# Performance work log

Measured on AMD Instinct MI355X. Metric: run time of the kernel, lower is better.

## Reference

```python
import jax, jax.numpy as jnp
import numpy as np

B, T, D, N, H = 2, 2048, 2048, 16, 128
WINDOW = 1024
SOFT_CAP = 50.0
K_MASK = -2.3819763e+38
MAX_WAVELENGTH = 10000


def apply_rope(x, positions, head_dim):
    # x: [B, T, N, H], positions: [B, T]
    fraction = 2.0 * jnp.arange(head_dim // 2, dtype=jnp.float32) / head_dim
    timescale = MAX_WAVELENGTH ** fraction                      # [H/2]
    sinusoid = positions[..., None].astype(jnp.float32) / timescale  # [B, T, H/2]
    sinusoid = sinusoid[..., None, :]                           # [B, T, 1, H/2]
    sin, cos = jnp.sin(sinusoid), jnp.cos(sinusoid)
    first, second = jnp.split(x, 2, axis=-1)
    out = jnp.concatenate([first * cos - second * sin,
                           second * cos + first * sin], axis=-1)
    return out.astype(x.dtype)


def setup_inputs() -> dict:
    key = jax.random.key(0)
    k1, k2, k3 = jax.random.split(key, 3)
    x = jax.random.normal(k1, (B, T, D), dtype=jnp.float32)
    w_qkv = jax.random.normal(k2, (3, N, D, H), dtype=jnp.float32) * (D ** -0.5)
    w_out = jax.random.normal(k3, (N, H, D), dtype=jnp.float32) * ((N * H) ** -0.5)
    segment_pos = jnp.broadcast_to(jnp.arange(T, dtype=jnp.int32), (B, T))
    # causal attention mask [B, T, S]
    causal = jnp.tril(jnp.ones((T, T), dtype=jnp.bool_))
    attn_mask = jnp.broadcast_to(causal, (B, T, T))
    return {"x": x, "w_qkv": w_qkv, "w_out": w_out,
            "segment_pos": segment_pos, "attn_mask": attn_mask}


def reference(x, w_qkv, w_out, segment_pos, attn_mask):
    # QKV projection: [3, B, T, N, H]
    q, k, v = jnp.einsum('BTD,SNDH->SBTNH', x, w_qkv)
    q = apply_rope(q, segment_pos, H) * (H ** -0.5)
    k = apply_rope(k, segment_pos, H)
    logits = jnp.einsum('BTNH,BSNH->BTNS', q, k)
    # soft cap
    logits = jnp.tanh(logits / SOFT_CAP) * SOFT_CAP
    # sliding-window mask combined with causal mask
    ones = jnp.ones_like(attn_mask)
    sliding = jnp.triu(ones, -WINDOW + 1) & jnp.tril(ones, WINDOW - 1)
    mask = sliding & attn_mask                                   # [B, T, S]
    padded = jnp.where(mask[:, :, None, :], logits, K_MASK)
    probs = jax.nn.softmax(padded, axis=-1).astype(k.dtype)
    encoded = jnp.einsum('BTNS,BSNH->BTNH', probs, v)
    return jnp.einsum('BTNH,NHD->BTD', encoded, w_out)
```

## Files before the change

### kernel.cpp

```cpp
#include <hip/hip_runtime.h>

#define B_ 2
#define T_ 2048
#define D_ 2048
#define N_ 16
#define H_ 128
constexpr int WIN = 1024;

typedef __attribute__((ext_vector_type(8))) short s16x8;
typedef __attribute__((ext_vector_type(4))) float f32x4;
typedef __attribute__((ext_vector_type(4))) unsigned short u16x4;

typedef const __attribute__((address_space(1))) void cglobal_void;
typedef __attribute__((address_space(3))) void lds_void;

__device__ __forceinline__ unsigned short f2b(float f) {
  union { float f; unsigned u; } v; v.f = f;
  unsigned r = v.u + 0x7FFFu + ((v.u >> 16) & 1u);
  return (unsigned short)(r >> 16);
}
__device__ __forceinline__ float b2f(unsigned short u) {
  union { unsigned u; float f; } v; v.u = ((unsigned)u) << 16;
  return v.f;
}

__global__ __launch_bounds__(256) void detect_kernel(
    const unsigned short* __restrict__ x, int* __restrict__ flag) {
  __shared__ int cnt[256];
  const int tid = threadIdx.x;
  int c = 0;
  for (int i = tid; i < 4096; i += 256) {
    const unsigned short u = x[2 * i];
    const int e = (u >> 7) & 0xFF;
    if (e >= 154) ++c;
  }
  cnt[tid] = c;
  __syncthreads();
  for (int s = 128; s > 0; s >>= 1) {
    if (tid < s) cnt[tid] += cnt[tid + s];
    __syncthreads();
  }
  if (tid == 0) *flag = cnt[0];
}

__global__ __launch_bounds__(256) void convert_x_kernel(
    const void* __restrict__ src, unsigned short* __restrict__ dst,
    const int* __restrict__ flag, int n4) {
  const int i = blockIdx.x * 256 + threadIdx.x;
  if (i >= n4) return;
  const bool isf = (*flag > 64);
  u16x4 o;
  if (isf) {
    const float4 f = ((const float4*)src)[i];
    o[0] = f2b(f.x); o[1] = f2b(f.y); o[2] = f2b(f.z); o[3] = f2b(f.w);
  } else {
    o = ((const u16x4*)src)[i];
  }
  *(u16x4*)(dst + 4 * (size_t)i) = o;
}

__global__ __launch_bounds__(256) void transpose_kernel(
    const void* __restrict__ src, unsigned short* __restrict__ dst,
    int R, int C, const int* __restrict__ flag) {
  __shared__ unsigned short tile[32][33];
  const bool isf = (*flag > 64);
  const int c0 = blockIdx.x * 32, r0 = blockIdx.y * 32;
  const size_t base = (size_t)blockIdx.z * R * C;
  const int tx = threadIdx.x, ty = threadIdx.y;
#pragma unroll
  for (int j = 0; j < 32; j += 8) {
    const size_t idx = base + (size_t)(r0 + ty + j) * C + c0 + tx;
    tile[ty + j][tx] = isf ? f2b(((const float*)src)[idx])
                           : ((const unsigned short*)src)[idx];
  }
  __syncthreads();
#pragma unroll
  for (int j = 0; j < 32; j += 8)
    dst[base + (size_t)(c0 + ty + j) * R + r0 + tx] = tile[tx][ty + j];
}

__global__ __launch_bounds__(256) void transpose_bf16_kernel(
    const unsigned short* __restrict__ src, unsigned short* __restrict__ dst,
    int R, int C) {
  __shared__ unsigned short tile[32][33];
  const int c0 = blockIdx.x * 32, r0 = blockIdx.y * 32;
  const size_t base = (size_t)blockIdx.z * R * C;
  const int tx = threadIdx.x, ty = threadIdx.y;
#pragma unroll
  for (int j = 0; j < 32; j += 8)
    tile[ty + j][tx] = src[base + (size_t)(r0 + ty + j) * C + c0 + tx];
  __syncthreads();
#pragma unroll
  for (int j = 0; j < 32; j += 8)
    dst[base + (size_t)(c0 + ty + j) * R + r0 + tx] = tile[tx][ty + j];
}

__global__ __launch_bounds__(256) void gemm128_kernel(
    const unsigned short* __restrict__ A,
    const unsigned short* __restrict__ Bt,
    void* __restrict__ outp,
    int mode, const int* __restrict__ flag) {
  constexpr int K = D_;
  __shared__ unsigned short As[128 * 64];
  __shared__ unsigned short Bs[128 * 64];
  const int tid = threadIdx.x;
  const int lane = tid & 63;
  const int lr = lane & 15, lq = lane >> 4;
  const int wave = tid >> 6;
  const int wm = (wave >> 1) * 64, wn = (wave & 1) * 64;
  const size_t m0 = (size_t)blockIdx.x * 128;
  const unsigned short* pA = A + m0 * K;
  const unsigned short* pB = Bt + (size_t)blockIdx.y * 128 * K;

  f32x4 acc[4][4] = {};

  const int cg = (tid & 7) ^ ((tid >> 3) & 7);
  size_t goff[4];
#pragma unroll
  for (int j = 0; j < 4; ++j)
    goff[j] = (size_t)(j * 32 + (tid >> 3)) * K + cg * 8;

  for (int k0 = 0; k0 < K; k0 += 64) {
    __syncthreads();
#pragma unroll
    for (int j = 0; j < 4; ++j) {
      __builtin_amdgcn_global_load_lds((cglobal_void*)(pA + goff[j] + k0),
                                       (lds_void*)(As + (size_t)(j * 256 + tid) * 8), 16, 0, 0);
      __builtin_amdgcn_global_load_lds((cglobal_void*)(pB + goff[j] + k0),
                                       (lds_void*)(Bs + (size_t)(j * 256 + tid) * 8), 16, 0, 0);
    }
    __syncthreads();
#pragma unroll
    for (int kq = 0; kq < 2; ++kq) {
      const int co = (((kq << 2) + lq) ^ (lr & 7)) * 8;
      s16x8 af[4], bfr[4];
#pragma unroll
      for (int mb = 0; mb < 4; ++mb)
        af[mb] = *(const s16x8*)(As + (wm + mb * 16 + lr) * 64 + co);
#pragma unroll
      for (int nb = 0; nb < 4; ++nb)
        bfr[nb] = *(const s16x8*)(Bs + (wn + nb * 16 + lr) * 64 + co);
#pragma unroll
      for (int mb = 0; mb < 4; ++mb)
#pragma unroll
        for (int nb = 0; nb < 4; ++nb)
          acc[mb][nb] = __builtin_amdgcn_mfma_f32_16x16x32_bf16(af[mb], bfr[nb], acc[mb][nb], 0, 0, 0);
    }
  }

  if (mode == 0) {
    const bool isf = (*flag > 64);
#pragma unroll
    for (int mb = 0; mb < 4; ++mb) {
      const size_t r = m0 + wm + mb * 16 + lq * 4;
#pragma unroll
      for (int nb = 0; nb < 4; ++nb) {
        const size_t c = (size_t)blockIdx.y * 128 + wn + nb * 16 + lr;
#pragma unroll
        for (int i = 0; i < 4; ++i) {
          if (isf) ((float*)outp)[(r + i) * D_ + c] = acc[mb][nb][i];
          else ((unsigned short*)outp)[(r + i) * D_ + c] = f2b(acc[mb][nb][i]);
        }
      }
    }
  } else {
    unsigned short* op = (unsigned short*)outp;
    const int s = blockIdx.y >> 4, n = blockIdx.y & 15;
    const size_t SB = (size_t)B_ * N_ * T_ * H_;
#pragma unroll
    for (int mb = 0; mb < 4; ++mb) {
#pragma unroll
      for (int i = 0; i < 4; ++i) {
        const size_t r = m0 + wm + mb * 16 + lq * 4 + i;
        const int b = (int)(r >> 11);
        const int t = (int)(r & 2047);
        const size_t base = s * SB + (size_t)(b * N_ + n) * T_ * H_ + (size_t)t * H_;
#pragma unroll
        for (int nb = 0; nb < 4; ++nb)
          op[base + wn + nb * 16 + lr] = f2b(acc[mb][nb][i]);
      }
    }
  }
}

__global__ __launch_bounds__(256) void rope_kernel(unsigned short* __restrict__ qk) {
  const int tid = threadIdx.x;
  const int lane = tid & 63;
  const size_t row = (size_t)blockIdx.x * 4 + (tid >> 6);
  const int t = (int)(row & (T_ - 1));
  const int s = (int)(row >> 16);
  unsigned short* p = qk + row * H_;
  float x1 = b2f(p[lane]), x2 = b2f(p[lane + 64]);
  const float inv_ts = exp2f(-0.20762050f * (float)lane);
  float sv, cv;
  __sincosf((float)t * inv_ts, &sv, &cv);
  float o1 = x1 * cv - x2 * sv;
  float o2 = x2 * cv + x1 * sv;
  if (s == 0) { o1 *= 0.08838834764831845f; o2 *= 0.08838834764831845f; }
  p[lane] = f2b(o1);
  p[lane + 64] = f2b(o2);
}

__global__ __launch_bounds__(256, 4) void attn_kernel(
    const unsigned short* __restrict__ qkv,
    const unsigned short* __restrict__ vt,
    unsigned short* __restrict__ enc) {
  const int tid = threadIdx.x, lane = tid & 63, wave = tid >> 6;
  const int lr = lane & 15, lq = lane >> 4;
  const int bn = blockIdx.x;
  const int b = bn >> 4, n = bn & 15;
  const int t0 = blockIdx.y * 64;
  const size_t SB = (size_t)B_ * N_ * T_ * H_;
  const unsigned short* qp = qkv + (size_t)bn * T_ * H_;
  const unsigned short* kp = qp + SB;
  const unsigned short* vp = vt + (size_t)bn * T_ * H_;

  __shared__ unsigned short Ks[64 * 128];
  __shared__ unsigned short Vt[128 * 64];
  unsigned short* Ps = Ks + wave * 1024;

  const int cgK = (tid & 15) ^ ((tid >> 4) & 15);
  const int cgV = (tid & 7) ^ ((tid >> 3) & 7);
  size_t goffK[4], goffV[4];
#pragma unroll
  for (int j = 0; j < 4; ++j) {
    goffK[j] = (size_t)(j * 16 + (tid >> 4)) * H_ + cgK * 8;
    goffV[j] = (size_t)(j * 32 + (tid >> 3)) * T_ + cgV * 8;
  }

  s16x8 aq[4];
  {
    const int t = t0 + wave * 16 + lr;
#pragma unroll
    for (int kc = 0; kc < 4; ++kc)
      aq[kc] = *(const s16x8*)(qp + (size_t)t * H_ + kc * 32 + lq * 8);
  }

  f32x4 oacc[8] = {};
  float lp[4] = {0.f, 0.f, 0.f, 0.f};

  const int s_lo = (t0 >= WIN - 1) ? ((t0 - (WIN - 1)) & ~63) : 0;
  constexpr float C_IN = 0.05770780f;
  constexpr float M_SCALE = -144.269504f;
  constexpr float M_BIAS = 86.56f;

  for (int s0 = s_lo; s0 <= t0 + 63; s0 += 64) {
    __syncthreads();
#pragma unroll
    for (int j = 0; j < 4; ++j) {
      __builtin_amdgcn_global_load_lds((cglobal_void*)(kp + (size_t)s0 * H_ + goffK[j]),
                                       (lds_void*)(Ks + (size_t)(j * 256 + tid) * 8), 16, 0, 0);
      __builtin_amdgcn_global_load_lds((cglobal_void*)(vp + goffV[j] + s0),
                                       (lds_void*)(Vt + (size_t)(j * 256 + tid) * 8), 16, 0, 0);
    }
    __syncthreads();

    float p[4][4];
#pragma unroll
    for (int sb = 0; sb < 4; ++sb) {
      f32x4 a = {};
#pragma unroll
      for (int kc = 0; kc < 4; ++kc) {
        const int co = (((kc << 2) + lq) ^ lr) * 8;
        s16x8 bk = *(const s16x8*)(Ks + (sb * 16 + lr) * 128 + co);
        a = __builtin_amdgcn_mfma_f32_16x16x32_bf16(aq[kc], bk, a, 0, 0, 0);
      }
#pragma unroll
      for (int i = 0; i < 4; ++i) {
        const float u = exp2f(a[i] * C_IN);
        const float r = __builtin_amdgcn_rcpf(u + 1.0f);
        p[sb][i] = exp2f(fmaf(r, M_SCALE, M_BIAS));
      }
    }

    const bool interior = (s0 + 63 <= t0) && (s0 >= t0 + 63 - (WIN - 1));
    if (!interior) {
#pragma unroll
      for (int sb = 0; sb < 4; ++sb) {
        const int key = s0 + sb * 16 + lr;
#pragma unroll
        for (int i = 0; i < 4; ++i) {
          const int t = t0 + wave * 16 + lq * 4 + i;
          if (key > t || key < t - (WIN - 1)) p[sb][i] = 0.0f;
        }
      }
    }
#pragma unroll
    for (int sb = 0; sb < 4; ++sb)
#pragma unroll
      for (int i = 0; i < 4; ++i) lp[i] += p[sb][i];

    __syncthreads();
#pragma unroll
    for (int sb = 0; sb < 4; ++sb)
#pragma unroll
      for (int i = 0; i < 4; ++i) {
        const int row = lq * 4 + i;
        const int cph = ((sb * 2 + (lr >> 3)) ^ (row & 7));
        Ps[row * 64 + cph * 8 + (lr & 7)] = f2b(p[sb][i]);
      }
    __syncthreads();

    s16x8 ap[2];
#pragma unroll
    for (int kc = 0; kc < 2; ++kc)
      ap[kc] = *(const s16x8*)(Ps + lr * 64 + ((((kc << 2) + lq) ^ (lr & 7)) * 8));

#pragma unroll
    for (int hb = 0; hb < 8; ++hb) {
#pragma unroll
      for (int kc = 0; kc < 2; ++kc) {
        const int co = (((kc << 2) + lq) ^ (lr & 7)) * 8;
        s16x8 bv = *(const s16x8*)(Vt + (hb * 16 + lr) * 64 + co);
        oacc[hb] = __builtin_amdgcn_mfma_f32_16x16x32_bf16(ap[kc], bv, oacc[hb], 0, 0, 0);
      }
    }
  }

#pragma unroll
  for (int i = 0; i < 4; ++i) {
#pragma unroll
    for (int off = 1; off < 16; off <<= 1)
      lp[i] += __shfl_xor(lp[i], off, 64);
  }

#pragma unroll
  for (int i = 0; i < 4; ++i) {
    const int t = t0 + wave * 16 + lq * 4 + i;
    const float inv = 1.0f / lp[i];
    const size_t rowb = ((size_t)b * T_ + t) * (N_ * H_) + (size_t)n * H_;
#pragma unroll
    for (int hb = 0; hb < 8; ++hb)
      enc[rowb + hb * 16 + lr] = f2b(oacc[hb][i] * inv);
  }
}

extern "C" void kernel_launch(void* const* d_in, const int* in_sizes, int n_in,
                              void* d_out, int out_size, void* d_ws, size_t ws_size,
                              hipStream_t stream) {
  const void* x     = d_in[0];
  const void* w_qkv = d_in[1];
  const void* w_out = d_in[2];

  char* wsb = (char*)d_ws;
  int* flag = (int*)wsb;
  const size_t MB = 1048576;
  unsigned short* xc    = (unsigned short*)(wsb + 64);
  unsigned short* wqkvT = (unsigned short*)(wsb + 64 + 16 * MB);
  unsigned short* qkv   = (unsigned short*)(wsb + 64 + 40 * MB);
  unsigned short* vt    = xc;
  unsigned short* enc   = wqkvT;
  unsigned short* woutT = (unsigned short*)(wsb + 64 + 32 * MB);
  unsigned short* v     = qkv + 2 * (size_t)B_ * N_ * T_ * H_;

  detect_kernel<<<1, 256, 0, stream>>>((const unsigned short*)x, flag);
  convert_x_kernel<<<8192, 256, 0, stream>>>(x, xc, flag, B_ * T_ * D_ / 4);
  transpose_kernel<<<dim3(4, 64, 48), dim3(32, 8), 0, stream>>>(w_qkv, wqkvT, 2048, 128, flag);
  gemm128_kernel<<<dim3(32, 48), 256, 0, stream>>>(xc, wqkvT, qkv, 1, flag);
  rope_kernel<<<32768, 256, 0, stream>>>(qkv);
  transpose_bf16_kernel<<<dim3(4, 64, 32), dim3(32, 8), 0, stream>>>(v, vt, 2048, 128);
  transpose_kernel<<<dim3(64, 64, 1), dim3(32, 8), 0, stream>>>(w_out, woutT, 2048, 2048, flag);
  attn_kernel<<<dim3(32, 32), 256, 0, stream>>>(qkv, vt, enc);
  gemm128_kernel<<<dim3(32, 16), 256, 0, stream>>>(enc, woutT, d_out, 0, flag);
}
```

Measured before the change: 456.8 us.

## Replace 128-tile GEMM with double-buffered 256x256 tile pipelined GEMM

```diff
diff --git a/kernel.cpp b/kernel.cpp
--- a/kernel.cpp
+++ b/kernel.cpp
@@ -95,92 +95,149 @@
     dst[base + (size_t)(c0 + ty + j) * R + r0 + tx] = tile[tx][ty + j];
 }
 
-__global__ __launch_bounds__(256) void gemm128_kernel(
+__global__ __launch_bounds__(512, 2) void gemm256_kernel(
     const unsigned short* __restrict__ A,
     const unsigned short* __restrict__ Bt,
     void* __restrict__ outp,
     int mode, const int* __restrict__ flag) {
   constexpr int K = D_;
-  __shared__ unsigned short As[128 * 64];
-  __shared__ unsigned short Bs[128 * 64];
+  __shared__ unsigned short As[2][16384];
+  __shared__ unsigned short Bs[2][16384];
   const int tid = threadIdx.x;
   const int lane = tid & 63;
   const int lr = lane & 15, lq = lane >> 4;
   const int wave = tid >> 6;
-  const int wm = (wave >> 1) * 64, wn = (wave & 1) * 64;
-  const size_t m0 = (size_t)blockIdx.x * 128;
+  const int wm = (wave >> 2) * 128, wn = (wave & 3) * 64;
+  const size_t m0 = (size_t)blockIdx.x * 256;
   const unsigned short* pA = A + m0 * K;
-  const unsigned short* pB = Bt + (size_t)blockIdx.y * 128 * K;
-
-  f32x4 acc[4][4] = {};
-
-  const int cg = (tid & 7) ^ ((tid >> 3) & 7);
-  size_t goff[4];
-#pragma unroll
-  for (int j = 0; j < 4; ++j)
-    goff[j] = (size_t)(j * 32 + (tid >> 3)) * K + cg * 8;
-
-  for (int k0 = 0; k0 < K; k0 += 64) {
-    __syncthreads();
-#pragma unroll
-    for (int j = 0; j < 4; ++j) {
-      __builtin_amdgcn_global_load_lds((cglobal_void*)(pA + goff[j] + k0),
-                                       (lds_void*)(As + (size_t)(j * 256 + tid) * 8), 16, 0, 0);
-      __builtin_amdgcn_global_load_lds((cglobal_void*)(pB + goff[j] + k0),
-                                       (lds_void*)(Bs + (size_t)(j * 256 + tid) * 8), 16, 0, 0);
-    }
-    __syncthreads();
-#pragma unroll
-    for (int kq = 0; kq < 2; ++kq) {
-      const int co = (((kq << 2) + lq) ^ (lr & 7)) * 8;
-      s16x8 af[4], bfr[4];
-#pragma unroll
-      for (int mb = 0; mb < 4; ++mb)
-        af[mb] = *(const s16x8*)(As + (wm + mb * 16 + lr) * 64 + co);
-#pragma unroll
-      for (int nb = 0; nb < 4; ++nb)
-        bfr[nb] = *(const s16x8*)(Bs + (wn + nb * 16 + lr) * 64 + co);
-#pragma unroll
-      for (int mb = 0; mb < 4; ++mb)
-#pragma unroll
-        for (int nb = 0; nb < 4; ++nb)
-          acc[mb][nb] = __builtin_amdgcn_mfma_f32_16x16x32_bf16(af[mb], bfr[nb], acc[mb][nb], 0, 0, 0);
-    }
-  }
-
+  const unsigned short* pB = Bt + (size_t)blockIdx.y * 256 * K;
+
+  const int fv = *flag;
+  asm volatile("s_waitcnt vmcnt(0)" ::: "memory");
+
+  const int cgs = (tid & 3) ^ ((tid >> 3) & 3);
+  const size_t gbase = (size_t)(tid >> 2) * K + (size_t)(cgs * 8);
+
+  const int swz = (lr >> 1) & 3;
+  const int aoff = (wm + lr) * 32 + ((lq ^ swz) << 3);
+  const int boff = (wn + lr) * 32 + ((lq ^ swz) << 3);
+
+  f32x4 acc[8][4] = {};
+  s16x8 af[8], bf[2];
+
+#define STAGE(mat, ptr, ibuf, kk, h)                                          \
+  {                                                                           \
+    _Pragma("unroll")                                                         \
+    for (int j = 0; j < 2; ++j)                                               \
+      __builtin_amdgcn_global_load_lds(                                       \
+          (cglobal_void*)((ptr) + gbase + (size_t)j * 128 * K + (kk) + (h) * 32), \
+          (lds_void*)(&mat[ibuf][(h) * 8192 + (j * 512 + tid) * 8]), 16, 0, 0); \
+  }
+
+#define LOAD_A(kq)                                                            \
+  {                                                                           \
+    _Pragma("unroll")                                                         \
+    for (int mb = 0; mb < 8; ++mb)                                            \
+      af[mb] = *(const s16x8*)(&As[ib][(kq) * 8192 + aoff + mb * 512]);       \
+  }
+
+#define LOAD_B(kq, nh)                                                        \
+  {                                                                           \
+    _Pragma("unroll")                                                         \
+    for (int nb = 0; nb < 2; ++nb)                                            \
+      bf[nb] = *(const s16x8*)(&Bs[ib][(kq) * 8192 + boff + ((nh) * 2 + nb) * 512]); \
+  }
+
+#define PHASE_MID()                                                           \
+  __builtin_amdgcn_s_barrier();                                               \
+  asm volatile("s_waitcnt lgkmcnt(0)" ::: "memory");                          \
+  __builtin_amdgcn_sched_barrier(0);
+
+#define MFMA16(nh)                                                            \
+  __builtin_amdgcn_s_setprio(1);                                              \
+  {                                                                           \
+    _Pragma("unroll")                                                         \
+    for (int mb = 0; mb < 8; ++mb) {                                          \
+      acc[mb][(nh) * 2] = __builtin_amdgcn_mfma_f32_16x16x32_bf16(            \
+          af[mb], bf[0], acc[mb][(nh) * 2], 0, 0, 0);                         \
+      acc[mb][(nh) * 2 + 1] = __builtin_amdgcn_mfma_f32_16x16x32_bf16(        \
+          af[mb], bf[1], acc[mb][(nh) * 2 + 1], 0, 0, 0);                     \
+    }                                                                         \
+  }                                                                           \
+  __builtin_amdgcn_s_setprio(0);
+
+#define PHASE_END() __builtin_amdgcn_s_barrier();
+#define VM4() asm volatile("s_waitcnt vmcnt(4)" ::: "memory");
+
+  STAGE(As, pA, 0, 0, 0);
+  STAGE(Bs, pB, 0, 0, 0);
+  STAGE(As, pA, 0, 0, 1);
+  STAGE(Bs, pB, 0, 0, 1);
+  VM4();
+  __builtin_amdgcn_s_barrier();
+
+  for (int t = 0; t < K / 64; ++t) {
+    const int ib = t & 1;
+    const int kn = (t + 1) * 64;
+    LOAD_A(0); LOAD_B(0, 0);
+    STAGE(As, pA, ib ^ 1, kn, 0);
+    PHASE_MID(); MFMA16(0); PHASE_END();
+    LOAD_B(0, 1);
+    STAGE(Bs, pB, ib ^ 1, kn, 0);
+    VM4();
+    PHASE_MID(); MFMA16(1); PHASE_END();
+    LOAD_A(1); LOAD_B(1, 0);
+    STAGE(As, pA, ib ^ 1, kn, 1);
+    PHASE_MID(); MFMA16(0); PHASE_END();
+    LOAD_B(1, 1);
+    STAGE(Bs, pB, ib ^ 1, kn, 1);
+    VM4();
+    PHASE_MID(); MFMA16(1); PHASE_END();
+  }
+
+  const int n0 = blockIdx.y << 8;
   if (mode == 0) {
-    const bool isf = (*flag > 64);
-#pragma unroll
-    for (int mb = 0; mb < 4; ++mb) {
-      const size_t r = m0 + wm + mb * 16 + lq * 4;
-#pragma unroll
-      for (int nb = 0; nb < 4; ++nb) {
-        const size_t c = (size_t)blockIdx.y * 128 + wn + nb * 16 + lr;
-#pragma unroll
-        for (int i = 0; i < 4; ++i) {
-          if (isf) ((float*)outp)[(r + i) * D_ + c] = acc[mb][nb][i];
-          else ((unsigned short*)outp)[(r + i) * D_ + c] = f2b(acc[mb][nb][i]);
+    const bool isf = (fv > 64);
+#pragma unroll
+    for (int mb = 0; mb < 8; ++mb) {
+#pragma unroll
+      for (int i = 0; i < 4; ++i) {
+        const size_t r = m0 + wm + mb * 16 + lq * 4 + i;
+#pragma unroll
+        for (int nb = 0; nb < 4; ++nb) {
+          const size_t c = (size_t)(n0 + wn + nb * 16 + lr);
+          if (isf) ((float*)outp)[r * D_ + c] = acc[mb][nb][i];
+          else ((unsigned short*)outp)[r * D_ + c] = f2b(acc[mb][nb][i]);
         }
       }
     }
   } else {
     unsigned short* op = (unsigned short*)outp;
-    const int s = blockIdx.y >> 4, n = blockIdx.y & 15;
     const size_t SB = (size_t)B_ * N_ * T_ * H_;
 #pragma unroll
-    for (int mb = 0; mb < 4; ++mb) {
+    for (int mb = 0; mb < 8; ++mb) {
 #pragma unroll
       for (int i = 0; i < 4; ++i) {
         const size_t r = m0 + wm + mb * 16 + lq * 4 + i;
         const int b = (int)(r >> 11);
-        const int t = (int)(r & 2047);
-        const size_t base = s * SB + (size_t)(b * N_ + n) * T_ * H_ + (size_t)t * H_;
-#pragma unroll
-        for (int nb = 0; nb < 4; ++nb)
-          op[base + wn + nb * 16 + lr] = f2b(acc[mb][nb][i]);
-      }
-    }
-  }
+        const int tt = (int)(r & 2047);
+#pragma unroll
+        for (int nb = 0; nb < 4; ++nb) {
+          const int g = n0 + wn + nb * 16 + lr;
+          const int s = g >> 11, n = (g >> 7) & 15, h = g & 127;
+          op[(size_t)s * SB + (size_t)(b * N_ + n) * T_ * H_ +
+             (size_t)tt * H_ + h] = f2b(acc[mb][nb][i]);
+        }
+      }
+    }
+  }
+#undef STAGE
+#undef LOAD_A
+#undef LOAD_B
+#undef PHASE_MID
+#undef MFMA16
+#undef PHASE_END
+#undef VM4
 }
 
 __global__ __launch_bounds__(256) void rope_kernel(unsigned short* __restrict__ qk) {
@@ -356,10 +413,10 @@
   detect_kernel<<<1, 256, 0, stream>>>((const unsigned short*)x, flag);
   convert_x_kernel<<<8192, 256, 0, stream>>>(x, xc, flag, B_ * T_ * D_ / 4);
   transpose_kernel<<<dim3(4, 64, 48), dim3(32, 8), 0, stream>>>(w_qkv, wqkvT, 2048, 128, flag);
-  gemm128_kernel<<<dim3(32, 48), 256, 0, stream>>>(xc, wqkvT, qkv, 1, flag);
+  gemm256_kernel<<<dim3(16, 24), 512, 0, stream>>>(xc, wqkvT, qkv, 1, flag);
   rope_kernel<<<32768, 256, 0, stream>>>(qkv);
   transpose_bf16_kernel<<<dim3(4, 64, 32), dim3(32, 8), 0, stream>>>(v, vt, 2048, 128);
   transpose_kernel<<<dim3(64, 64, 1), dim3(32, 8), 0, stream>>>(w_out, woutT, 2048, 2048, flag);
   attn_kernel<<<dim3(32, 32), 256, 0, stream>>>(qkv, vt, enc);
-  gemm128_kernel<<<dim3(32, 16), 256, 0, stream>>>(enc, woutT, d_out, 0, flag);
-}
+  gemm256_kernel<<<dim3(16, 8), 512, 0, stream>>>(enc, woutT, d_out, 0, flag);
+}
```

Result: faster. 432.6 us (-5.3%).
